# Performance work log

Measured on AMD Instinct MI355X. Metric: run time of the kernel, lower is better.

## Reference

```python
import jax, jax.numpy as jnp
import numpy as np

DIM, HEADS, DIM_HEAD = 256, 8, 32  # dim == heads * dim_head
EPS = 1e-5


def setup_inputs() -> dict:
    key = jax.random.key(0)
    ks = jax.random.split(key, 6)
    B, C, H, W = 16, DIM, 64, 64
    x = jax.random.normal(ks[0], (B, C, H, W), dtype=jnp.float32)
    # 1x1 conv weights stored as [out_ch, in_ch]
    w_qkv = jax.random.normal(ks[1], (3 * DIM, DIM), dtype=jnp.float32) * (1.0 / np.sqrt(DIM))
    w_out = jax.random.normal(ks[2], (DIM, DIM), dtype=jnp.float32) * (1.0 / np.sqrt(DIM))
    b_out = jax.random.normal(ks[3], (DIM,), dtype=jnp.float32) * 0.01
    ln_gamma = jnp.ones((DIM,), dtype=jnp.float32)
    ln_beta = jnp.zeros((DIM,), dtype=jnp.float32)
    return {"x": x, "w_qkv": w_qkv, "w_out": w_out, "b_out": b_out,
            "ln_gamma": ln_gamma, "ln_beta": ln_beta}


def _linear_attention(x, w_qkv, w_out, b_out, ln_gamma, ln_beta):
    B, C, H, W = x.shape
    d = C // HEADS
    # 1x1 conv == channel matmul
    qkv = jnp.einsum('bchw,oc->bohw', x, w_qkv)  # [B, 3C, H, W]
    q, k, v = jnp.split(qkv, 3, axis=1)
    # 'b (h d) x y -> b h x y d'
    def split_heads(t):
        t = t.reshape(B, HEADS, d, H, W)
        return t.transpose(0, 1, 3, 4, 2)  # b h x y d
    q, k, v = split_heads(q), split_heads(k), split_heads(v)
    q = jax.nn.softmax(q, axis=-1)   # over d (channel) dim
    k = jax.nn.softmax(k, axis=-2)   # over y spatial axis (faithful to torch dim=-2)
    context = jnp.einsum('bhxyd,bhxye->bhde', k, v)          # [B,H,d,d]
    out = jnp.einsum('bhde,bhxye->bhxyd', context, q)        # [B,H,X,Y,d]
    # 'b h x y d -> b (h d) x y'
    out = out.transpose(0, 1, 4, 2, 3).reshape(B, C, H, W)
    # output 1x1 conv + bias
    out = jnp.einsum('bchw,oc->bohw', out, w_out) + b_out[None, :, None, None]
    # LayerNorm over channel dim (permute to NHWC, norm last axis, permute back)
    y = out.transpose(0, 2, 3, 1)  # b h w c
    mu = jnp.mean(y, axis=-1, keepdims=True)
    var = jnp.var(y, axis=-1, keepdims=True)
    y = (y - mu) / jnp.sqrt(var + EPS) * ln_gamma + ln_beta
    return y.transpose(0, 3, 1, 2)


def reference(x, w_qkv, w_out, b_out, ln_gamma, ln_beta):
    return _linear_attention(x, w_qkv, w_out, b_out, ln_gamma, ln_beta)
```

## Files before the change

kernel.cpp:

```cpp
#include <hip/hip_runtime.h>
#include <hip/hip_bf16.h>

#define NB 16
#define CDIM 256
#define NHEADS 8
#define DH 32
#define NSP 4096
#define O3 768

typedef __bf16 bf16;
typedef bf16 bf16x4 __attribute__((ext_vector_type(4)));
typedef bf16 bf16x8 __attribute__((ext_vector_type(8)));
typedef float f32x4 __attribute__((ext_vector_type(4)));
typedef float f32x16 __attribute__((ext_vector_type(16)));

static __device__ __forceinline__ float bf2f(bf16 x){ return (float)x; }
static __device__ __forceinline__ bf16 f2bf(float x){ return (bf16)x; }

static __device__ __forceinline__ void gld16(const bf16* g, bf16* l){
    __builtin_amdgcn_global_load_lds((const __attribute__((address_space(1))) void*)g,
                                     (__attribute__((address_space(3))) void*)l, 16, 0, 0);
}

__global__ void k_transpose(const float* __restrict__ x, bf16* __restrict__ xT){
    __shared__ bf16 tile[64][72];
    int b = blockIdx.z;
    int c0 = blockIdx.y * 64;
    int n0 = blockIdx.x * 64;
    int t = threadIdx.x;
    const float* xb = x + (size_t)b * CDIM * NSP;
    #pragma unroll
    for (int i = 0; i < 4; ++i){
        int lin = i*256 + t;
        int c = lin >> 4;
        int n4 = (lin & 15) * 4;
        f32x4 f = *(const f32x4*)(xb + (size_t)(c0 + c)*NSP + n0 + n4);
        bf16x4 v4;
        #pragma unroll
        for (int j = 0; j < 4; ++j) v4[j] = f2bf(f[j]);
        *(bf16x4*)&tile[c][n4] = v4;
    }
    __syncthreads();
    bf16* xTb = xT + (size_t)b * NSP * CDIM;
    #pragma unroll
    for (int i = 0; i < 2; ++i){
        int lin = i*256 + t;
        int n = lin >> 3;
        int c8 = (lin & 7) * 8;
        bf16x8 v;
        #pragma unroll
        for (int j = 0; j < 8; ++j) v[j] = tile[c8+j][n];
        *(bf16x8*)(xTb + (size_t)(n0+n)*CDIM + c0 + c8) = v;
    }
}

__global__ void k_wcvt(const float* __restrict__ w, bf16* __restrict__ w2){
    int idx = (blockIdx.x*256 + threadIdx.x) * 4;
    f32x4 f = *(const f32x4*)(w + idx);
    bf16x4 v;
    #pragma unroll
    for (int j=0;j<4;j++) v[j] = f2bf(f[j]);
    *(bf16x4*)(w2 + idx) = v;
}

__global__ __launch_bounds__(1024,4) void k_kvctx(const bf16* __restrict__ w2,
                                                  const bf16* __restrict__ xT,
                                                  float* __restrict__ ctx_p){
    __shared__ union {
        bf16 Bs[32768];
        bf16 cb[32768];
    } sm;
    int bid = blockIdx.x;
    int xcd = bid & 7, slot = bid >> 3;
    int g = xcd*64 + slot;
    int b = g >> 5;
    int ntile = g & 31;
    int n0 = ntile * 128;
    int t = threadIdx.x;
    int wv = t >> 6, lane = t & 63;

    #pragma unroll
    for (int j=0;j<4;j++){
        int base_r = wv*8 + j*2;
        int r = base_r + (lane>>5);
        int c = (lane & 31) ^ (r & 7);
        gld16(xT + ((size_t)b*NSP + n0 + r)*CDIM + c*8, &sm.Bs[(size_t)base_r*256]);
    }
    __syncthreads();

    int brow[8], brx[8];
    #pragma unroll
    for (int ni=0;ni<8;ni++){
        int r = ni*16 + (lane&15);
        brow[ni] = r*32; brx[ni] = r & 7;
    }
    int arow = 256 + wv*32 + (lane&15);
    int acol = (lane>>4)*8;

    f32x4 acc[2][8];
    #pragma unroll
    for (int i=0;i<16;i++) ((f32x4*)acc)[i] = (f32x4){0.f,0.f,0.f,0.f};

    bf16x8 af0 = *(const bf16x8*)(w2 + (size_t)(arow     )*CDIM + acol);
    bf16x8 af1 = *(const bf16x8*)(w2 + (size_t)(arow + 16)*CDIM + acol);
    #pragma unroll
    for (int k0=0;k0<8;k0++){
        bf16x8 an0, an1;
        if (k0 < 7){
            an0 = *(const bf16x8*)(w2 + (size_t)(arow     )*CDIM + (k0+1)*32 + acol);
            an1 = *(const bf16x8*)(w2 + (size_t)(arow + 16)*CDIM + (k0+1)*32 + acol);
        }
        int cbase = (lane>>4) + k0*4;
        bf16x8 bfr[8];
        #pragma unroll
        for (int ni=0;ni<8;ni++)
            bfr[ni] = *(const bf16x8*)&sm.Bs[(size_t)(brow[ni] + (cbase ^ brx[ni]))*8];
        #pragma unroll
        for (int ni=0;ni<8;ni++)
            acc[0][ni] = __builtin_amdgcn_mfma_f32_16x16x32_bf16(af0, bfr[ni], acc[0][ni], 0, 0, 0);
        #pragma unroll
        for (int ni=0;ni<8;ni++)
            acc[1][ni] = __builtin_amdgcn_mfma_f32_16x16x32_bf16(af1, bfr[ni], acc[1][ni], 0, 0, 0);
        af0 = an0; af1 = an1;
    }

    if (wv < 8){
        #pragma unroll
        for (int mi=0;mi<2;mi++)
            #pragma unroll
            for (int r=0;r<4;r++)
                #pragma unroll
                for (int grp=0;grp<2;grp++){
                    float mx = -1e30f;
                    #pragma unroll
                    for (int q=0;q<4;q++) mx = fmaxf(mx, acc[mi][grp*4+q][r]);
                    #pragma unroll
                    for (int msk=1; msk<16; msk<<=1) mx = fmaxf(mx, __shfl_xor(mx, msk, 64));
                    float s = 0.f;
                    #pragma unroll
                    for (int q=0;q<4;q++){
                        float e = __expf(acc[mi][grp*4+q][r] - mx);
                        acc[mi][grp*4+q][r] = e; s += e;
                    }
                    #pragma unroll
                    for (int msk=1; msk<16; msk<<=1) s += __shfl_xor(s, msk, 64);
                    float inv = 1.f/s;
                    #pragma unroll
                    for (int q=0;q<4;q++) acc[mi][grp*4+q][r] *= inv;
                }
    }

    #pragma unroll
    for (int ph=0; ph<2; ++ph){
        __syncthreads();
        if (((wv>>2)&1) == ph){
            int isv  = wv >> 3;
            int w03  = wv & 3;
            int base = isv * 16384;
            #pragma unroll
            for (int mi=0;mi<2;mi++)
                #pragma unroll
                for (int ni=0;ni<8;ni++)
                    #pragma unroll
                    for (int r=0;r<4;r++){
                        int row = w03*32 + mi*16 + (lane>>4)*4 + r;
                        int n = ni*16 + (lane&15);
                        sm.cb[base + row*128 + (((n>>3) ^ (row&15))<<3) + (n&7)] = f2bf(acc[mi][ni][r]);
                    }
        }
        __syncthreads();
        if (wv < 4){
            f32x16 cacc;
            #pragma unroll
            for (int i=0;i<16;i++) cacc[i] = 0.f;
            int rr = wv*32 + (lane&31);
            #pragma unroll
            for (int s=0;s<8;s++){
                int nseg = s*2 + (lane>>5);
                int off = rr*128 + (((nseg ^ (rr&15))<<3));
                bf16x8 ka = *(const bf16x8*)&sm.cb[off];
                bf16x8 vb = *(const bf16x8*)&sm.cb[16384 + off];
                cacc = __builtin_amdgcn_mfma_f32_32x32x16_bf16(ka, vb, cacc, 0, 0, 0);
            }
            float* dst = ctx_p + ((size_t)(b*8 + ph*4 + wv)*32 + ntile)*1024;
            #pragma unroll
            for (int r=0;r<16;r++){
                int d = (r&3) + 8*(r>>2) + 4*(lane>>5);
                dst[d*32 + (lane&31)] = cacc[r];
            }
        }
    }
}

__global__ void k_merge(const float* __restrict__ w_out, const float* __restrict__ ctx_p,
                        bf16* __restrict__ W2){
    __shared__ float ctxs[32][32];
    int bh = blockIdx.x;
    int b = bh >> 3, h = bh & 7;
    int t = threadIdx.x;
    const float* base = ctx_p + (size_t)bh*32*1024;
    #pragma unroll
    for (int i=0;i<4;i++){
        int idx = i*256 + t;
        float s0 = 0.f, s1 = 0.f;
        #pragma unroll
        for (int p=0;p<16;p++){ s0 += base[(2*p)*1024 + idx]; s1 += base[(2*p+1)*1024 + idx]; }
        ((float*)ctxs)[idx] = s0 + s1;
    }
    __syncthreads();
    int o = t;
    const float* wrow = w_out + (size_t)o*CDIM + h*DH;
    float wv[32];
    #pragma unroll
    for (int d=0;d<32;d++) wv[d] = wrow[d];
    bf16* dst = W2 + ((size_t)b*CDIM + o)*CDIM + h*DH;
    #pragma unroll
    for (int g=0;g<4;g++){
        bf16x8 o8;
        #pragma unroll
        for (int jj=0;jj<8;jj++){
            int e = g*8 + jj;
            float s = 0.f;
            #pragma unroll
            for (int d=0;d<32;d++) s += wv[d]*ctxs[d][e];
            o8[jj] = f2bf(s);
        }
        *(bf16x8*)(dst + g*8) = o8;
    }
}

__global__ __launch_bounds__(256,4) void k_qout_ln(const bf16* __restrict__ w2,
                                                   const bf16* __restrict__ xT,
                                                   const bf16* __restrict__ W2,
                                                   const float* __restrict__ bout,
                                                   const float* __restrict__ gamma,
                                                   const float* __restrict__ beta,
                                                   float* __restrict__ out){
    __shared__ union {
        bf16 Bs[8192];
        float Y[256*33];
    } sm;
    __shared__ float red[2][8][32];
    __shared__ float mu_s[32], rstd_s[32];
    int bid = blockIdx.x;
    int xcd = bid & 7, slot = bid >> 3;
    int b  = slot >> 4;
    int n0 = (xcd*16 + (slot & 15)) * 32;
    int t = threadIdx.x, wv = t>>6, lane = t&63;

    const bf16* xTb = xT + (size_t)b * NSP * CDIM;
    #pragma unroll
    for (int j=0;j<4;j++){
        int base_r = wv*8 + j*2;
        int r = base_r + (lane>>5);
        int c = (lane & 31) ^ (r & 7);
        gld16(xTb + (size_t)(n0 + r)*CDIM + c*8, &sm.Bs[(size_t)base_r*256]);
    }
    __syncthreads();

    int brow[2], brx[2];
    #pragma unroll
    for (int ni=0;ni<2;ni++){
        int r = ni*16 + (lane&15);
        brow[ni] = r*32; brx[ni] = r & 7;
    }
    int arow = wv*64 + (lane&15);
    int acol = (lane>>4)*8;

    f32x4 acc[4][2];
    #pragma unroll
    for (int i=0;i<8;i++) ((f32x4*)acc)[i] = (f32x4){0.f,0.f,0.f,0.f};
    {
        bf16x8 af[4], an[4];
        #pragma unroll
        for (int mi=0;mi<4;mi++)
            af[mi] = *(const bf16x8*)(w2 + (size_t)(arow + mi*16)*CDIM + acol);
        #pragma unroll
        for (int k0=0;k0<8;k0++){
            if (k0 < 7){
                #pragma unroll
                for (int mi=0;mi<4;mi++)
                    an[mi] = *(const bf16x8*)(w2 + (size_t)(arow + mi*16)*CDIM + (k0+1)*32 + acol);
            }
            int cbase = (lane>>4) + k0*4;
            bf16x8 bfr[2];
            #pragma unroll
            for (int ni=0;ni<2;ni++)
                bfr[ni] = *(const bf16x8*)&sm.Bs[(size_t)(brow[ni] + (cbase ^ brx[ni]))*8];
            #pragma unroll
            for (int mi=0;mi<4;mi++)
                #pragma unroll
                for (int ni=0;ni<2;ni++)
                    acc[mi][ni] = __builtin_amdgcn_mfma_f32_16x16x32_bf16(af[mi], bfr[ni], acc[mi][ni], 0, 0, 0);
            #pragma unroll
            for (int mi=0;mi<4;mi++) af[mi] = an[mi];
        }
    }

    #pragma unroll
    for (int ni=0;ni<2;ni++)
        #pragma unroll
        for (int hp=0;hp<2;hp++){
            float mx = -1e30f;
            #pragma unroll
            for (int mi=2*hp; mi<2*hp+2; mi++)
                #pragma unroll
                for (int r=0;r<4;r++) mx = fmaxf(mx, acc[mi][ni][r]);
            mx = fmaxf(mx, __shfl_xor(mx, 16, 64));
            mx = fmaxf(mx, __shfl_xor(mx, 32, 64));
            float s = 0.f;
            #pragma unroll
            for (int mi=2*hp; mi<2*hp+2; mi++)
                #pragma unroll
                for (int r=0;r<4;r++){
                    float e = __expf(acc[mi][ni][r] - mx);
                    acc[mi][ni][r] = e; s += e;
                }
            s += __shfl_xor(s, 16, 64);
            s += __shfl_xor(s, 32, 64);
            float inv = 1.f/s;
            #pragma unroll
            for (int mi=2*hp; mi<2*hp+2; mi++)
                #pragma unroll
                for (int r=0;r<4;r++) acc[mi][ni][r] *= inv;
        }

    __syncthreads();
    #pragma unroll
    for (int mi=0;mi<4;mi++)
        #pragma unroll
        for (int ni=0;ni<2;ni++){
            int n_loc = ni*16 + (lane&15);
            int cseg  = wv*8 + mi*2 + (lane>>5);
            bf16x4 v4;
            #pragma unroll
            for (int r=0;r<4;r++) v4[r] = f2bf(acc[mi][ni][r]);
            *(bf16x4*)&sm.Bs[(size_t)(n_loc*32 + (cseg ^ (n_loc&7)))*8 + ((lane>>4)&1)*4] = v4;
        }
    __syncthreads();

    const bf16* Ab = W2 + (size_t)b*CDIM*CDIM;
    f32x4 acc2[4][2];
    #pragma unroll
    for (int i=0;i<8;i++) ((f32x4*)acc2)[i] = (f32x4){0.f,0.f,0.f,0.f};
    {
        bf16x8 af[4], an[4];
        #pragma unroll
        for (int mi=0;mi<4;mi++)
            af[mi] = *(const bf16x8*)(Ab + (size_t)(arow + mi*16)*CDIM + acol);
        #pragma unroll
        for (int k0=0;k0<8;k0++){
            if (k0 < 7){
                #pragma unroll
                for (int mi=0;mi<4;mi++)
                    an[mi] = *(const bf16x8*)(Ab + (size_t)(arow + mi*16)*CDIM + (k0+1)*32 + acol);
            }
            int cbase = (lane>>4) + k0*4;
            bf16x8 bfr[2];
            #pragma unroll
            for (int ni=0;ni<2;ni++)
                bfr[ni] = *(const bf16x8*)&sm.Bs[(size_t)(brow[ni] + (cbase ^ brx[ni]))*8];
            #pragma unroll
            for (int mi=0;mi<4;mi++)
                #pragma unroll
                for (int ni=0;ni<2;ni++)
                    acc2[mi][ni] = __builtin_amdgcn_mfma_f32_16x16x32_bf16(af[mi], bfr[ni], acc2[mi][ni], 0, 0, 0);
            #pragma unroll
            for (int mi=0;mi<4;mi++) af[mi] = an[mi];
        }
    }

    __syncthreads();
    #pragma unroll
    for (int mi=0;mi<4;mi++)
        #pragma unroll
        for (int ni=0;ni<2;ni++)
            #pragma unroll
            for (int r=0;r<4;r++){
                int o = wv*64 + mi*16 + (lane>>4)*4 + r;
                int n = ni*16 + (lane&15);
                sm.Y[o*33 + n] = acc2[mi][ni][r];
            }
    __syncthreads();
    int n = t & 31, q = t >> 5;
    float s = 0.f, s2 = 0.f;
    for (int o=32*q; o<32*q+32; o++){
        float y = sm.Y[o*33+n] + bout[o];
        s += y; s2 += y*y;
    }
    red[0][q][n] = s; red[1][q][n] = s2;
    __syncthreads();
    if (t < 32){
        float S = 0.f, S2 = 0.f;
        #pragma unroll
        for (int p=0;p<8;p++){ S += red[0][p][t]; S2 += red[1][p][t]; }
        float mu = S * (1.f/256.f);
        float var = S2*(1.f/256.f) - mu*mu;
        mu_s[t] = mu; rstd_s[t] = rsqrtf(var + 1e-5f);
    }
    __syncthreads();
    float mu = mu_s[n], rstd = rstd_s[n];
    size_t ob = (size_t)b*CDIM*NSP + n0 + n;
    for (int o=32*q; o<32*q+32; o++){
        float y = sm.Y[o*33+n] + bout[o];
        out[ob + (size_t)o*NSP] = (y - mu)*rstd*gamma[o] + beta[o];
    }
}

extern "C" void kernel_launch(void* const* d_in, const int* in_sizes, int n_in,
                              void* d_out, int out_size, void* d_ws, size_t ws_size,
                              hipStream_t stream){
    const float* x     = (const float*)d_in[0];
    const float* w_qkv = (const float*)d_in[1];
    const float* w_out = (const float*)d_in[2];
    const float* b_out = (const float*)d_in[3];
    const float* gamma = (const float*)d_in[4];
    const float* beta  = (const float*)d_in[5];
    float* out = (float*)d_out;
    char* ws = (char*)d_ws;
    bf16*  xT    = (bf16*) ws;
    float* ctx_p = (float*)(ws + 67108864ull);
    bf16*  W2    = (bf16*)(ws + 134742016ull);
    bf16*  w2    = (bf16*)(ws + 136839168ull);

    k_wcvt     <<<dim3(192),       256,  0, stream>>>(w_qkv, w2);
    k_transpose<<<dim3(64, 4, NB), 256,  0, stream>>>(x, xT);
    k_kvctx    <<<dim3(512),       1024, 0, stream>>>(w2, xT, ctx_p);
    k_merge    <<<dim3(128),       256,  0, stream>>>(w_out, ctx_p, W2);
    k_qout_ln  <<<dim3(2048),      256,  0, stream>>>(w2, xT, W2, b_out, gamma, beta, out);
}
```

Baseline: 237.9 us.

## Compute LayerNorm from MFMA registers instead of staging through shared memory

The LayerNorm epilogue now takes its statistics straight from the accumulator registers, using cross-lane shuffles and a small per-wave reduction. This removes the large float Y staging buffer and its two extra barriers, so shared memory per block drops to the 16 KB bf16 tile, and launch bounds are raised to 8 blocks per CU. Output stores now go directly from the MFMA layout, so each wave writes 16-element contiguous runs instead of 32, which may make stores less coalesced. The tighter launch bound may also force register spills.

```diff
diff --git a/kernel.cpp b/kernel.cpp
--- a/kernel.cpp
+++ b/kernel.cpp
@@ -229,18 +229,15 @@
     }
 }
 
-__global__ __launch_bounds__(256,4) void k_qout_ln(const bf16* __restrict__ w2,
+__global__ __launch_bounds__(256,8) void k_qout_ln(const bf16* __restrict__ w2,
                                                    const bf16* __restrict__ xT,
                                                    const bf16* __restrict__ W2,
                                                    const float* __restrict__ bout,
                                                    const float* __restrict__ gamma,
                                                    const float* __restrict__ beta,
                                                    float* __restrict__ out){
-    __shared__ union {
-        bf16 Bs[8192];
-        float Y[256*33];
-    } sm;
-    __shared__ float red[2][8][32];
+    __shared__ bf16 Bs[8192];
+    __shared__ float red[2][4][2][16];
     __shared__ float mu_s[32], rstd_s[32];
     int bid = blockIdx.x;
     int xcd = bid & 7, slot = bid >> 3;
@@ -254,7 +251,7 @@
         int base_r = wv*8 + j*2;
         int r = base_r + (lane>>5);
         int c = (lane & 31) ^ (r & 7);
-        gld16(xTb + (size_t)(n0 + r)*CDIM + c*8, &sm.Bs[(size_t)base_r*256]);
+        gld16(xTb + (size_t)(n0 + r)*CDIM + c*8, &Bs[(size_t)base_r*256]);
     }
     __syncthreads();
 
@@ -286,7 +283,7 @@
             bf16x8 bfr[2];
             #pragma unroll
             for (int ni=0;ni<2;ni++)
-                bfr[ni] = *(const bf16x8*)&sm.Bs[(size_t)(brow[ni] + (cbase ^ brx[ni]))*8];
+                bfr[ni] = *(const bf16x8*)&Bs[(size_t)(brow[ni] + (cbase ^ brx[ni]))*8];
             #pragma unroll
             for (int mi=0;mi<4;mi++)
                 #pragma unroll
@@ -335,7 +332,7 @@
             bf16x4 v4;
             #pragma unroll
             for (int r=0;r<4;r++) v4[r] = f2bf(acc[mi][ni][r]);
-            *(bf16x4*)&sm.Bs[(size_t)(n_loc*32 + (cseg ^ (n_loc&7)))*8 + ((lane>>4)&1)*4] = v4;
+            *(bf16x4*)&Bs[(size_t)(n_loc*32 + (cseg ^ (n_loc&7)))*8 + ((lane>>4)&1)*4] = v4;
         }
     __syncthreads();
 
@@ -359,7 +356,7 @@
             bf16x8 bfr[2];
             #pragma unroll
             for (int ni=0;ni<2;ni++)
-                bfr[ni] = *(const bf16x8*)&sm.Bs[(size_t)(brow[ni] + (cbase ^ brx[ni]))*8];
+                bfr[ni] = *(const bf16x8*)&Bs[(size_t)(brow[ni] + (cbase ^ brx[ni]))*8];
             #pragma unroll
             for (int mi=0;mi<4;mi++)
                 #pragma unroll
@@ -370,40 +367,61 @@
         }
     }
 
-    __syncthreads();
-    #pragma unroll
-    for (int mi=0;mi<4;mi++)
+    float sA[2] = {0.f, 0.f}, sB[2] = {0.f, 0.f};
+    #pragma unroll
+    for (int mi=0;mi<4;mi++){
+        f32x4 b4 = *(const f32x4*)&bout[wv*64 + mi*16 + (lane>>4)*4];
         #pragma unroll
         for (int ni=0;ni<2;ni++)
             #pragma unroll
             for (int r=0;r<4;r++){
-                int o = wv*64 + mi*16 + (lane>>4)*4 + r;
-                int n = ni*16 + (lane&15);
-                sm.Y[o*33 + n] = acc2[mi][ni][r];
-            }
-    __syncthreads();
-    int n = t & 31, q = t >> 5;
-    float s = 0.f, s2 = 0.f;
-    for (int o=32*q; o<32*q+32; o++){
-        float y = sm.Y[o*33+n] + bout[o];
-        s += y; s2 += y*y;
-    }
-    red[0][q][n] = s; red[1][q][n] = s2;
+                float y = acc2[mi][ni][r] + b4[r];
+                acc2[mi][ni][r] = y;
+                sA[ni] += y; sB[ni] += y*y;
+            }
+    }
+    #pragma unroll
+    for (int ni=0;ni<2;ni++){
+        sA[ni] += __shfl_xor(sA[ni], 16, 64); sA[ni] += __shfl_xor(sA[ni], 32, 64);
+        sB[ni] += __shfl_xor(sB[ni], 16, 64); sB[ni] += __shfl_xor(sB[ni], 32, 64);
+    }
+    if (lane < 16){
+        #pragma unroll
+        for (int ni=0;ni<2;ni++){
+            red[0][wv][ni][lane] = sA[ni];
+            red[1][wv][ni][lane] = sB[ni];
+        }
+    }
     __syncthreads();
     if (t < 32){
         float S = 0.f, S2 = 0.f;
         #pragma unroll
-        for (int p=0;p<8;p++){ S += red[0][p][t]; S2 += red[1][p][t]; }
+        for (int w=0;w<4;w++){ S += red[0][w][t>>4][t&15]; S2 += red[1][w][t>>4][t&15]; }
         float mu = S * (1.f/256.f);
         float var = S2*(1.f/256.f) - mu*mu;
         mu_s[t] = mu; rstd_s[t] = rsqrtf(var + 1e-5f);
     }
     __syncthreads();
-    float mu = mu_s[n], rstd = rstd_s[n];
-    size_t ob = (size_t)b*CDIM*NSP + n0 + n;
-    for (int o=32*q; o<32*q+32; o++){
-        float y = sm.Y[o*33+n] + bout[o];
-        out[ob + (size_t)o*NSP] = (y - mu)*rstd*gamma[o] + beta[o];
+    float mu[2], rs[2];
+    #pragma unroll
+    for (int ni=0;ni<2;ni++){
+        mu[ni] = mu_s[ni*16 + (lane&15)];
+        rs[ni] = rstd_s[ni*16 + (lane&15)];
+    }
+    size_t obase = (size_t)b*CDIM*NSP + n0 + (lane&15);
+    #pragma unroll
+    for (int mi=0;mi<4;mi++){
+        int o0 = wv*64 + mi*16 + (lane>>4)*4;
+        f32x4 g4  = *(const f32x4*)&gamma[o0];
+        f32x4 be4 = *(const f32x4*)&beta[o0];
+        #pragma unroll
+        for (int r=0;r<4;r++){
+            #pragma unroll
+            for (int ni=0;ni<2;ni++){
+                float yv = (acc2[mi][ni][r] - mu[ni])*rs[ni]*g4[r] + be4[r];
+                out[obase + (size_t)(o0 + r)*NSP + ni*16] = yv;
+            }
+        }
     }
 }
 
```

Result: slower. 288.3 us (+21.2%).
